# Kernel tuning notes

Measured on AMD Instinct MI355X. Metric: run time of the kernel, lower is better.

Reference implementation:

```python
import jax, jax.numpy as jnp
import numpy as np

N_NODES = 100000
N_EDGES = 150000
D_IN = 512
D_HID = 512
N_GRAPHS = 64


def setup_inputs() -> dict:
    key = jax.random.key(0)
    ks = jax.random.split(key, 12)
    x = jax.random.normal(ks[0], (N_NODES, D_IN), dtype=jnp.float32)
    edge_index = jax.random.randint(ks[1], (2, N_EDGES), 0, N_NODES, dtype=jnp.int64)
    batch = jnp.sort(jax.random.randint(ks[2], (N_NODES,), 0, N_GRAPHS, dtype=jnp.int64))
    s1 = 1.0 / np.sqrt(D_IN)
    s2 = 1.0 / np.sqrt(D_HID)
    # GINConv layer 1: MLP([D_IN, D_HID, D_HID])
    W1a = jax.random.uniform(ks[3], (D_IN, D_HID), jnp.float32, -s1, s1)
    b1a = jax.random.uniform(ks[4], (D_HID,), jnp.float32, -s1, s1)
    W1b = jax.random.uniform(ks[5], (D_HID, D_HID), jnp.float32, -s2, s2)
    b1b = jax.random.uniform(ks[6], (D_HID,), jnp.float32, -s2, s2)
    # GINConv layer 2 (out_channels=1): MLP([D_HID, 1, 1])
    W2a = jax.random.uniform(ks[7], (D_HID, 1), jnp.float32, -s2, s2)
    b2a = jax.random.uniform(ks[8], (1,), jnp.float32, -s2, s2)
    W2b = jax.random.uniform(ks[9], (1, 1), jnp.float32, -1.0, 1.0)
    b2b = jax.random.uniform(ks[10], (1,), jnp.float32, -1.0, 1.0)
    return {"x": x, "edge_index": edge_index, "batch": batch,
            "W1a": W1a, "b1a": b1a, "W1b": W1b, "b1b": b1b,
            "W2a": W2a, "b2a": b2a, "W2b": W2b, "b2b": b2b}


def _gin_conv(h, src, dst, Wa, ba, Wb, bb):
    # sum-aggregate neighbor features, add (1+eps)*x with eps=0, then MLP
    agg = jax.ops.segment_sum(h[src], dst, num_segments=N_NODES)  # [N, d]
    z = agg + h
    z = jnp.maximum(jnp.dot(z, Wa) + ba, 0.0)  # Linear -> ReLU
    return jnp.dot(z, Wb) + bb                  # Linear (plain last)


def reference(x, edge_index, batch, W1a, b1a, W1b, b1b, W2a, b2a, W2b, b2b):
    src, dst = edge_index[0], edge_index[1]
    h = _gin_conv(x, src, dst, W1a, b1a, W1b, b1b)
    h = jnp.maximum(h, 0.0)  # inter-layer activation (not applied after last layer)
    h = _gin_conv(h, src, dst, W2a, b2a, W2b, b2b)  # [N, 1]
    # global mean pool over graph assignment
    sums = jax.ops.segment_sum(h, batch, num_segments=N_GRAPHS)  # [G, 1]
    cnt = jax.ops.segment_sum(jnp.ones((N_NODES, 1), h.dtype), batch, num_segments=N_GRAPHS)
    return sums / jnp.maximum(cnt, 1.0)
```

## Files before the change

### kernel.cpp

```cpp
#include <hip/hip_runtime.h>
#include <hip/hip_bf16.h>

#define N_NODES_C 100000
#define N_EDGES_C 150000
#define DC 512
#define NG 64

typedef float f32x4 __attribute__((ext_vector_type(4)));
typedef short s16x8 __attribute__((ext_vector_type(8)));
typedef unsigned int u32;

__device__ __forceinline__ short f2bf(float f) {
    union { float f; unsigned u; } c; c.f = f;
    unsigned r = c.u + 0x7fffu + ((c.u >> 16) & 1u);
    return (short)(r >> 16);
}
__device__ __forceinline__ float bf2f(short v) {
    union { unsigned u; float f; } c;
    c.u = ((unsigned)(unsigned short)v) << 16;
    return c.f;
}

__device__ __forceinline__ void gload16(const void* g, void* l) {
    __builtin_amdgcn_global_load_lds((const __attribute__((address_space(1))) u32*)g,
                                     (__attribute__((address_space(3))) u32*)l,
                                     16, 0, 0);
}


__global__ void zero_k(float* s, float* aggs, int* cnt, float* gsum, float* gcnt) {
    int i = blockIdx.x * 256 + threadIdx.x;
    if (i < N_NODES_C) { s[i] = 0.f; aggs[i] = 0.f; cnt[i] = 0; }
    if (i < NG) { gsum[i] = 0.f; gcnt[i] = 0.f; }
}

__global__ void transpose_w(const float* __restrict__ in, short* __restrict__ out) {
    __shared__ float tile[32][33];
    int tx = threadIdx.x & 31;
    int ty = threadIdx.x >> 5;
    int k0 = blockIdx.y * 32;
    int n0 = blockIdx.x * 32;
#pragma unroll
    for (int i = 0; i < 4; ++i)
        tile[ty + i * 8][tx] = in[(size_t)(k0 + ty + i * 8) * DC + n0 + tx];
    __syncthreads();
#pragma unroll
    for (int i = 0; i < 4; ++i)
        out[(size_t)(n0 + ty + i * 8) * DC + k0 + tx] = f2bf(tile[tx][ty + i * 8]);
}


__global__ void hist_k(const int* __restrict__ ei, int* __restrict__ cnt) {
    int e = blockIdx.x * 256 + threadIdx.x;
    if (e < N_EDGES_C) atomicAdd(&cnt[ei[N_EDGES_C + e]], 1);
}

__global__ void scan1_k(const int* __restrict__ cnt, int* __restrict__ off,
                        int* __restrict__ bsum) {
    __shared__ int sh[1024];
    int tid = threadIdx.x;
    int i = blockIdx.x * 1024 + tid;
    int v = (i < N_NODES_C) ? cnt[i] : 0;
    sh[tid] = v;
    __syncthreads();
    for (int d = 1; d < 1024; d <<= 1) {
        int t = (tid >= d) ? sh[tid - d] : 0;
        __syncthreads();
        sh[tid] += t;
        __syncthreads();
    }
    if (i < N_NODES_C) off[i] = sh[tid] - v;
    if (tid == 1023) bsum[blockIdx.x] = sh[1023];
}

#define NSCAN_BLK 98

__global__ void scan2_k(int* __restrict__ bsum) {
    __shared__ int sh[128];
    int tid = threadIdx.x;
    int v = (tid < NSCAN_BLK) ? bsum[tid] : 0;
    sh[tid] = v;
    __syncthreads();
    for (int d = 1; d < 128; d <<= 1) {
        int t = (tid >= d) ? sh[tid - d] : 0;
        __syncthreads();
        sh[tid] += t;
        __syncthreads();
    }
    if (tid < NSCAN_BLK) bsum[tid] = sh[tid] - v;
}

__global__ void scan3_k(int* __restrict__ off, const int* __restrict__ bsum) {
    int i = blockIdx.x * 1024 + threadIdx.x;
    if (i < N_NODES_C) off[i] += bsum[blockIdx.x];
}

__global__ void place_k(const int* __restrict__ ei, int* __restrict__ off,
                        int* __restrict__ ssrc) {
    int e = blockIdx.x * 256 + threadIdx.x;
    if (e < N_EDGES_C) {
        int d = ei[N_EDGES_C + e];
        int p = atomicAdd(&off[d], 1);
        ssrc[p] = ei[e];
    }
}

__global__ void gather_relu_k(const short* __restrict__ y, const int* __restrict__ off,
                              const int* __restrict__ ssrc, const float* __restrict__ b1a,
                              short* __restrict__ z1) {
    int node = blockIdx.x * 4 + (threadIdx.x >> 6);
    if (node >= N_NODES_C) return;
    int t = threadIdx.x & 63;
    const int col = t * 8;
    int beg = (node == 0) ? 0 : off[node - 1];
    int end = off[node];
    s16x8 own = *(const s16x8*)(y + (size_t)node * DC + col);
    float acc[8];
#pragma unroll
    for (int q = 0; q < 8; ++q) acc[q] = bf2f(own[q]);
    int j = beg;
    for (; j + 2 <= end; j += 2) {
        int s0 = ssrc[j];
        int s1 = ssrc[j + 1];
        s16x8 r0 = *(const s16x8*)(y + (size_t)s0 * DC + col);
        s16x8 r1 = *(const s16x8*)(y + (size_t)s1 * DC + col);
#pragma unroll
        for (int q = 0; q < 8; ++q) acc[q] += bf2f(r0[q]) + bf2f(r1[q]);
    }
    if (j < end) {
        int s0 = ssrc[j];
        s16x8 r0 = *(const s16x8*)(y + (size_t)s0 * DC + col);
#pragma unroll
        for (int q = 0; q < 8; ++q) acc[q] += bf2f(r0[q]);
    }
    f32x4 bv0 = *(const f32x4*)(b1a + col);
    f32x4 bv1 = *(const f32x4*)(b1a + col + 4);
    s16x8 o;
    o[0] = f2bf(fmaxf(acc[0] + bv0.x, 0.f));
    o[1] = f2bf(fmaxf(acc[1] + bv0.y, 0.f));
    o[2] = f2bf(fmaxf(acc[2] + bv0.z, 0.f));
    o[3] = f2bf(fmaxf(acc[3] + bv0.w, 0.f));
    o[4] = f2bf(fmaxf(acc[4] + bv1.x, 0.f));
    o[5] = f2bf(fmaxf(acc[5] + bv1.y, 0.f));
    o[6] = f2bf(fmaxf(acc[6] + bv1.z, 0.f));
    o[7] = f2bf(fmaxf(acc[7] + bv1.w, 0.f));
    *(s16x8*)(z1 + (size_t)node * DC + col) = o;
}


__global__ void edge_scalar(const int* __restrict__ ei, const float* __restrict__ s,
                            float* __restrict__ aggs) {
    int e = blockIdx.x * 256 + threadIdx.x;
    if (e < N_EDGES_C) atomicAdd(&aggs[ei[N_EDGES_C + e]], s[ei[e]]);
}

__global__ void node_pool(const float* __restrict__ s, const float* __restrict__ aggs,
                          const int* __restrict__ batch, const float* __restrict__ b2a,
                          float* __restrict__ gsum, float* __restrict__ gcnt) {
    __shared__ float ls[NG], lc[NG];
    int t = threadIdx.x;
    if (t < NG) { ls[t] = 0.f; lc[t] = 0.f; }
    __syncthreads();
    int i = blockIdx.x * 256 + t;
    if (i < N_NODES_C) {
        float z2 = fmaxf(aggs[i] + s[i] + b2a[0], 0.0f);
        int g = batch[i];
        atomicAdd(&ls[g], z2);
        atomicAdd(&lc[g], 1.0f);
    }
    __syncthreads();
    if (t < NG && lc[t] != 0.f) {
        atomicAdd(&gsum[t], ls[t]);
        atomicAdd(&gcnt[t], lc[t]);
    }
}

__global__ void finalize_k(const float* gsum, const float* gcnt, const float* w2b,
                           const float* b2b, float* out) {
    int g = threadIdx.x;
    if (g < NG) {
        float c = fmaxf(gcnt[g], 1.0f);
        out[g] = gsum[g] / c * w2b[0] + b2b[0];
    }
}

#define BM 128
#define BN 128
#define BK 32
#define NKT (DC / BK)
#define NRB 782
#define NCB 4
#define NWG (NRB * NCB)
#define WG_PER_XCD (NWG / 8)

template <int ASRC, int EPI>
__global__ __launch_bounds__(256, 3) void gemm_k(const void* __restrict__ Ap,
                                                 const short* __restrict__ Bt,
                                                 const float* __restrict__ bias,
                                                 short* __restrict__ Cout,
                                                 const float* __restrict__ w2a,
                                                 float* __restrict__ s_out) {
    __shared__ alignas(16) short As[BM * BK];
    __shared__ alignas(16) short Bs[BN * BK];

    const int tid = threadIdx.x;
    const int bid = blockIdx.x;
    const int lin = (bid & 7) * WG_PER_XCD + (bid >> 3);
    const int brow = (lin >> 2) * BM;
    const int bcol = (lin & 3) * BN;

    const int w    = tid >> 6;
    const int lane = tid & 63;
    const int wr   = (w >> 1) * 64;
    const int wc   = (w & 1) * 64;
    const int lr   = lane & 15;
    const int lk   = (lane >> 4) * 8;

    f32x4 acc[4][4] = {};

    const int srow = lane >> 2;
    const int scol = (lane & 3) * 8;
    const short* bg0 = Bt + (size_t)(bcol + w * 32 + srow) * DC + scol;
    const short* bg1 = bg0 + (size_t)16 * DC;
    short* bl0 = &Bs[(w * 32) * BK];
    short* bl1 = &Bs[(w * 32 + 16) * BK];

    const short* ag0 = nullptr;
    const short* ag1 = nullptr;
    short* al0 = nullptr;
    short* al1 = nullptr;
    const float* af32 = nullptr;
    f32x4 areg[4];
    const int awrow = tid >> 1;
    const int awcol = (tid & 1) * 16;

    if constexpr (ASRC == 1) {
        int ar0 = brow + w * 32 + srow;
        int ar1 = ar0 + 16;
        if (ar0 >= N_NODES_C) ar0 = N_NODES_C - 1;
        if (ar1 >= N_NODES_C) ar1 = N_NODES_C - 1;
        ag0 = (const short*)Ap + (size_t)ar0 * DC + scol;
        ag1 = (const short*)Ap + (size_t)ar1 * DC + scol;
        al0 = &As[(w * 32) * BK];
        al1 = &As[(w * 32 + 16) * BK];
    } else {
        int ar = brow + awrow;
        if (ar >= N_NODES_C) ar = N_NODES_C - 1;
        af32 = (const float*)Ap + (size_t)ar * DC + awcol;
#pragma unroll
        for (int q = 0; q < 4; ++q) areg[q] = *(const f32x4*)(af32 + q * 4);
    }

    for (int kt = 0; kt < NKT; ++kt) {
        const int k0 = kt * BK;
        __syncthreads();
        if constexpr (ASRC == 1) {
            gload16(ag0 + k0, al0);
            gload16(ag1 + k0, al1);
        } else {
            s16x8 c0, c1;
            c0[0] = f2bf(areg[0].x); c0[1] = f2bf(areg[0].y);
            c0[2] = f2bf(areg[0].z); c0[3] = f2bf(areg[0].w);
            c0[4] = f2bf(areg[1].x); c0[5] = f2bf(areg[1].y);
            c0[6] = f2bf(areg[1].z); c0[7] = f2bf(areg[1].w);
            c1[0] = f2bf(areg[2].x); c1[1] = f2bf(areg[2].y);
            c1[2] = f2bf(areg[2].z); c1[3] = f2bf(areg[2].w);
            c1[4] = f2bf(areg[3].x); c1[5] = f2bf(areg[3].y);
            c1[6] = f2bf(areg[3].z); c1[7] = f2bf(areg[3].w);
            *(s16x8*)&As[awrow * BK + awcol + 0] = c0;
            *(s16x8*)&As[awrow * BK + awcol + 8] = c1;
        }
        gload16(bg0 + k0, bl0);
        gload16(bg1 + k0, bl1);
        __syncthreads();

        if constexpr (ASRC == 0) {
            if (kt + 1 < NKT) {
#pragma unroll
                for (int q = 0; q < 4; ++q)
                    areg[q] = *(const f32x4*)(af32 + (kt + 1) * BK + q * 4);
            }
        }

        s16x8 af[4], bfr[4];
#pragma unroll
        for (int mi = 0; mi < 4; ++mi)
            af[mi] = *(const s16x8*)&As[(wr + mi * 16 + lr) * BK + lk];
#pragma unroll
        for (int ni = 0; ni < 4; ++ni)
            bfr[ni] = *(const s16x8*)&Bs[(wc + ni * 16 + lr) * BK + lk];
        __builtin_amdgcn_s_setprio(1);
#pragma unroll
        for (int mi = 0; mi < 4; ++mi)
#pragma unroll
            for (int ni = 0; ni < 4; ++ni)
                acc[mi][ni] = __builtin_amdgcn_mfma_f32_16x16x32_bf16(af[mi], bfr[ni],
                                                                      acc[mi][ni], 0, 0, 0);
        __builtin_amdgcn_s_setprio(0);
    }

    const int rb = brow + wr + (lane >> 4) * 4;
    const int cb = bcol + wc + lr;

    if constexpr (EPI == 2) {
#pragma unroll
        for (int mi = 0; mi < 4; ++mi) {
#pragma unroll
            for (int r = 0; r < 4; ++r) {
                int row = rb + mi * 16 + r;
                if (row < N_NODES_C) {
#pragma unroll
                    for (int ni = 0; ni < 4; ++ni)
                        Cout[(size_t)row * DC + cb + ni * 16] = f2bf(acc[mi][ni][r]);
                }
            }
        }
    } else {
        float bv[4], wv[4];
#pragma unroll
        for (int ni = 0; ni < 4; ++ni) {
            bv[ni] = bias[cb + ni * 16];
            wv[ni] = w2a[cb + ni * 16];
        }
#pragma unroll
        for (int mi = 0; mi < 4; ++mi) {
#pragma unroll
            for (int r = 0; r < 4; ++r) {
                float sum = 0.f;
#pragma unroll
                for (int ni = 0; ni < 4; ++ni) {
                    float v = fmaxf(acc[mi][ni][r] + bv[ni], 0.0f);
                    sum += v * wv[ni];
                }
#pragma unroll
                for (int off = 1; off < 16; off <<= 1) sum += __shfl_xor(sum, off, 64);
                int row = rb + mi * 16 + r;
                if (lr == 0 && row < N_NODES_C) atomicAdd(&s_out[row], sum);
            }
        }
    }
}


extern "C" void kernel_launch(void* const* d_in, const int* in_sizes, int n_in,
                              void* d_out, int out_size, void* d_ws, size_t ws_size,
                              hipStream_t stream) {
    const float* x     = (const float*)d_in[0];
    const int*   ei    = (const int*)d_in[1];
    const int*   batch = (const int*)d_in[2];
    const float* W1a   = (const float*)d_in[3];
    const float* b1a   = (const float*)d_in[4];
    const float* W1b   = (const float*)d_in[5];
    const float* b1b   = (const float*)d_in[6];
    const float* W2a   = (const float*)d_in[7];
    const float* b2a   = (const float*)d_in[8];
    const float* W2b   = (const float*)d_in[9];
    const float* b2b   = (const float*)d_in[10];
    float* out = (float*)d_out;

    char* w = (char*)d_ws;
    short* z1   = (short*)(w);
    short* y    = (short*)(w + 102400000);
    short* WT1  = (short*)(w + 204800000);
    short* WT2  = (short*)(w + 205324288);
    float* sbuf = (float*)(w + 205848576);
    float* aggs = (float*)(w + 206248576);
    int*   cnt  = (int*)  (w + 206648576);
    int*   offb = (int*)  (w + 207048576);
    int*   ssrc = (int*)  (w + 207448576);
    int*   bsum = (int*)  (w + 208048576);
    float* gsum = (float*)(w + 208049088);
    float* gcnt = (float*)(w + 208049344);

    zero_k<<<391, 256, 0, stream>>>(sbuf, aggs, cnt, gsum, gcnt);
    transpose_w<<<dim3(16, 16), 256, 0, stream>>>(W1a, WT1);
    transpose_w<<<dim3(16, 16), 256, 0, stream>>>(W1b, WT2);

    hist_k<<<586, 256, 0, stream>>>(ei, cnt);
    scan1_k<<<NSCAN_BLK, 1024, 0, stream>>>(cnt, offb, bsum);
    scan2_k<<<1, 128, 0, stream>>>(bsum);
    scan3_k<<<NSCAN_BLK, 1024, 0, stream>>>(offb, bsum);
    place_k<<<586, 256, 0, stream>>>(ei, offb, ssrc);

    gemm_k<0, 2><<<NWG, 256, 0, stream>>>(x, WT1, nullptr, y, nullptr, nullptr);
    gather_relu_k<<<25000, 256, 0, stream>>>(y, offb, ssrc, b1a, z1);
    gemm_k<1, 1><<<NWG, 256, 0, stream>>>(z1, WT2, b1b, nullptr, W2a, sbuf);

    edge_scalar<<<586, 256, 0, stream>>>(ei, sbuf, aggs);
    node_pool<<<391, 256, 0, stream>>>(sbuf, aggs, batch, b2a, gsum, gcnt);
    finalize_k<<<1, 64, 0, stream>>>(gsum, gcnt, W2b, b2b, out);
}
```

Before: 297.4 us.

## Rewrite GEMM with 256x128 tiles, triple-buffered LDS and swizzled layout

Replaces the 128x128x32 double-sync GEMM with a 512-thread kernel using 256x128 tiles, BK=64, and a three-stage LDS ring buffer that prefetches two K-tiles ahead. Waits use explicit vmcnt counts and a single barrier per iteration. The LDS layout is XOR-swizzled to avoid bank conflicts. This is meant to hide global-load latency and cut barrier overhead, at the cost of 144KB of dynamic LDS, which limits occupancy to one workgroup per CU, plus hand-tuned waitcnt logic that is fragile.

```diff
diff --git a/kernel.cpp b/kernel.cpp
--- a/kernel.cpp
+++ b/kernel.cpp
@@ -184,123 +184,191 @@
     }
 }
 
-#define BM 128
-#define BN 128
-#define BK 32
-#define NKT (DC / BK)
-#define NRB 782
-#define NCB 4
-#define NWG (NRB * NCB)
-#define WG_PER_XCD (NWG / 8)
+#define NKT8 8
+#define BUF_SHORTS 24576
+#define LDS_BYTES (3 * BUF_SHORTS * 2)
+#define NWG8 1568
+#define WPX8 196
+
+#define VMCNT(n) asm volatile("s_waitcnt vmcnt(" #n ")")
+#define LGKM0() asm volatile("s_waitcnt lgkmcnt(0)")
+#define SCHEDB() __builtin_amdgcn_sched_barrier(0)
+#define HWBAR() __builtin_amdgcn_s_barrier()
 
 template <int ASRC, int EPI>
-__global__ __launch_bounds__(256, 3) void gemm_k(const void* __restrict__ Ap,
-                                                 const short* __restrict__ Bt,
-                                                 const float* __restrict__ bias,
-                                                 short* __restrict__ Cout,
-                                                 const float* __restrict__ w2a,
-                                                 float* __restrict__ s_out) {
-    __shared__ alignas(16) short As[BM * BK];
-    __shared__ alignas(16) short Bs[BN * BK];
+__global__ __launch_bounds__(512) void gemm8_k(const void* __restrict__ Ap,
+                                               const short* __restrict__ Bt,
+                                               const float* __restrict__ bias,
+                                               short* __restrict__ Cout,
+                                               const float* __restrict__ w2a,
+                                               float* __restrict__ s_out) {
+    extern __shared__ short lds[];
 
     const int tid = threadIdx.x;
     const int bid = blockIdx.x;
-    const int lin = (bid & 7) * WG_PER_XCD + (bid >> 3);
-    const int brow = (lin >> 2) * BM;
-    const int bcol = (lin & 3) * BN;
+    const int lin = (bid & 7) * WPX8 + (bid >> 3);
+    const int brow = (lin >> 2) * 256;
+    const int bcol = (lin & 3) * 128;
 
     const int w    = tid >> 6;
     const int lane = tid & 63;
-    const int wr   = (w >> 1) * 64;
-    const int wc   = (w & 1) * 64;
+    const int wm   = w >> 1;
+    const int wn   = w & 1;
     const int lr   = lane & 15;
-    const int lk   = (lane >> 4) * 8;
+    const int lg   = lane >> 4;
+    const int l3   = lane >> 3;
+    const int sc   = ((lane & 7) ^ l3) * 8;
 
     f32x4 acc[4][4] = {};
 
-    const int srow = lane >> 2;
-    const int scol = (lane & 3) * 8;
-    const short* bg0 = Bt + (size_t)(bcol + w * 32 + srow) * DC + scol;
-    const short* bg1 = bg0 + (size_t)16 * DC;
-    short* bl0 = &Bs[(w * 32) * BK];
-    short* bl1 = &Bs[(w * 32 + 16) * BK];
-
-    const short* ag0 = nullptr;
-    const short* ag1 = nullptr;
-    short* al0 = nullptr;
-    short* al1 = nullptr;
-    const float* af32 = nullptr;
-    f32x4 areg[4];
-    const int awrow = tid >> 1;
-    const int awcol = (tid & 1) * 16;
-
+    const short* bsrc0 = Bt + (size_t)(bcol + 0 * 64 + w * 8 + l3) * DC + sc;
+    const short* bsrc1 = Bt + (size_t)(bcol + 1 * 64 + w * 8 + l3) * DC + sc;
+    const int boff0 = 16384 + (0 * 64 + w * 8) * 64;
+    const int boff1 = 16384 + (1 * 64 + w * 8) * 64;
+
+    const short* asrc[4];
+    int aoff[4];
+    const float* axsrc = nullptr;
+    int awoff[4];
     if constexpr (ASRC == 1) {
-        int ar0 = brow + w * 32 + srow;
-        int ar1 = ar0 + 16;
-        if (ar0 >= N_NODES_C) ar0 = N_NODES_C - 1;
-        if (ar1 >= N_NODES_C) ar1 = N_NODES_C - 1;
-        ag0 = (const short*)Ap + (size_t)ar0 * DC + scol;
-        ag1 = (const short*)Ap + (size_t)ar1 * DC + scol;
-        al0 = &As[(w * 32) * BK];
-        al1 = &As[(w * 32 + 16) * BK];
+#pragma unroll
+        for (int i = 0; i < 4; ++i) {
+            int r = brow + i * 64 + w * 8 + l3;
+            if (r >= N_NODES_C) r = N_NODES_C - 1;
+            asrc[i] = (const short*)Ap + (size_t)r * DC + sc;
+            aoff[i] = (i * 64 + w * 8) * 64;
+        }
     } else {
-        int ar = brow + awrow;
-        if (ar >= N_NODES_C) ar = N_NODES_C - 1;
-        af32 = (const float*)Ap + (size_t)ar * DC + awcol;
-#pragma unroll
-        for (int q = 0; q < 4; ++q) areg[q] = *(const f32x4*)(af32 + q * 4);
-    }
-
-    for (int kt = 0; kt < NKT; ++kt) {
-        const int k0 = kt * BK;
-        __syncthreads();
-        if constexpr (ASRC == 1) {
-            gload16(ag0 + k0, al0);
-            gload16(ag1 + k0, al1);
+        const int rAl = tid >> 1;
+        int r = brow + rAl;
+        if (r >= N_NODES_C) r = N_NODES_C - 1;
+        axsrc = (const float*)Ap + (size_t)r * DC + (tid & 1) * 32;
+#pragma unroll
+        for (int j = 0; j < 4; ++j)
+            awoff[j] = rAl * 64 + ((((tid & 1) * 4 + j) ^ (rAl & 7)) * 8);
+    }
+
+#define STAGE_B(t, sb_)                                  \
+    do {                                                 \
+        short* _p = &lds[(sb_)*BUF_SHORTS];              \
+        gload16(bsrc0 + (t)*64, _p + boff0);             \
+        gload16(bsrc1 + (t)*64, _p + boff1);             \
+    } while (0)
+#define STAGE_A1(t, sb_)                                 \
+    do {                                                 \
+        short* _p = &lds[(sb_)*BUF_SHORTS];              \
+        gload16(asrc[0] + (t)*64, _p + aoff[0]);         \
+        gload16(asrc[1] + (t)*64, _p + aoff[1]);         \
+        gload16(asrc[2] + (t)*64, _p + aoff[2]);         \
+        gload16(asrc[3] + (t)*64, _p + aoff[3]);         \
+    } while (0)
+#define LOAD_A0(t, fr)                                                    \
+    _Pragma("unroll") for (int q = 0; q < 8; ++q)                         \
+        fr[q] = *(const f32x4*)(axsrc + (t)*64 + q * 4);
+#define WRITE_A0(sb_, fr)                                                 \
+    do {                                                                  \
+        short* _p = &lds[(sb_)*BUF_SHORTS];                               \
+        _Pragma("unroll") for (int j = 0; j < 4; ++j) {                   \
+            s16x8 _c;                                                     \
+            _c[0] = f2bf(fr[2 * j].x);     _c[1] = f2bf(fr[2 * j].y);     \
+            _c[2] = f2bf(fr[2 * j].z);     _c[3] = f2bf(fr[2 * j].w);     \
+            _c[4] = f2bf(fr[2 * j + 1].x); _c[5] = f2bf(fr[2 * j + 1].y); \
+            _c[6] = f2bf(fr[2 * j + 1].z); _c[7] = f2bf(fr[2 * j + 1].w); \
+            *(s16x8*)&_p[awoff[j]] = _c;                                  \
+        }                                                                 \
+    } while (0)
+
+    if constexpr (ASRC == 1) {
+        STAGE_A1(0, 0); STAGE_B(0, 0);
+        STAGE_A1(1, 1); STAGE_B(1, 1);
+        VMCNT(6);
+        SCHEDB();
+        HWBAR();
+    } else {
+        f32x4 p0[8], p1[8];
+        LOAD_A0(0, p0);
+        STAGE_B(0, 0);
+        LOAD_A0(1, p1);
+        STAGE_B(1, 1);
+        WRITE_A0(0, p0);
+        WRITE_A0(1, p1);
+        VMCNT(0);
+        LGKM0();
+        SCHEDB();
+        HWBAR();
+    }
+
+    int bufR = 0, bufS = 2;
+    for (int kt = 0; kt < NKT8; ++kt) {
+        const short* bp = &lds[bufR * BUF_SHORTS];
+
+        f32x4 fr[8];
+        if (kt < NKT8 - 2) {
+            if constexpr (ASRC == 1) {
+                STAGE_A1(kt + 2, bufS);
+                STAGE_B(kt + 2, bufS);
+            } else {
+                LOAD_A0(kt + 2, fr);
+                STAGE_B(kt + 2, bufS);
+            }
+            SCHEDB();
+        }
+
+#pragma unroll
+        for (int kk = 0; kk < 2; ++kk) {
+            s16x8 af[4], bfr[4];
+#pragma unroll
+            for (int mi = 0; mi < 4; ++mi)
+                af[mi] = *(const s16x8*)&bp[(wm * 64 + mi * 16 + lr) * 64 +
+                                            (((kk * 4 + lg) ^ (lr & 7)) * 8)];
+#pragma unroll
+            for (int ni = 0; ni < 4; ++ni)
+                bfr[ni] = *(const s16x8*)&bp[16384 + (wn * 64 + ni * 16 + lr) * 64 +
+                                             (((kk * 4 + lg) ^ (lr & 7)) * 8)];
+            __builtin_amdgcn_s_setprio(1);
+#pragma unroll
+            for (int mi = 0; mi < 4; ++mi)
+#pragma unroll
+                for (int ni = 0; ni < 4; ++ni)
+                    acc[mi][ni] = __builtin_amdgcn_mfma_f32_16x16x32_bf16(
+                        af[mi], bfr[ni], acc[mi][ni], 0, 0, 0);
+            __builtin_amdgcn_s_setprio(0);
+        }
+
+        if constexpr (ASRC == 0) {
+            if (kt < NKT8 - 2) {
+                VMCNT(2);
+                SCHEDB();
+                WRITE_A0(bufS, fr);
+                LGKM0();
+                SCHEDB();
+                HWBAR();
+            } else if (kt == NKT8 - 2) {
+                VMCNT(0);
+                SCHEDB();
+                HWBAR();
+            }
         } else {
-            s16x8 c0, c1;
-            c0[0] = f2bf(areg[0].x); c0[1] = f2bf(areg[0].y);
-            c0[2] = f2bf(areg[0].z); c0[3] = f2bf(areg[0].w);
-            c0[4] = f2bf(areg[1].x); c0[5] = f2bf(areg[1].y);
-            c0[6] = f2bf(areg[1].z); c0[7] = f2bf(areg[1].w);
-            c1[0] = f2bf(areg[2].x); c1[1] = f2bf(areg[2].y);
-            c1[2] = f2bf(areg[2].z); c1[3] = f2bf(areg[2].w);
-            c1[4] = f2bf(areg[3].x); c1[5] = f2bf(areg[3].y);
-            c1[6] = f2bf(areg[3].z); c1[7] = f2bf(areg[3].w);
-            *(s16x8*)&As[awrow * BK + awcol + 0] = c0;
-            *(s16x8*)&As[awrow * BK + awcol + 8] = c1;
-        }
-        gload16(bg0 + k0, bl0);
-        gload16(bg1 + k0, bl1);
-        __syncthreads();
-
-        if constexpr (ASRC == 0) {
-            if (kt + 1 < NKT) {
-#pragma unroll
-                for (int q = 0; q < 4; ++q)
-                    areg[q] = *(const f32x4*)(af32 + (kt + 1) * BK + q * 4);
+            if (kt < NKT8 - 2) {
+                VMCNT(6);
+                SCHEDB();
+                HWBAR();
+            } else if (kt == NKT8 - 2) {
+                VMCNT(0);
+                SCHEDB();
+                HWBAR();
             }
         }
-
-        s16x8 af[4], bfr[4];
-#pragma unroll
-        for (int mi = 0; mi < 4; ++mi)
-            af[mi] = *(const s16x8*)&As[(wr + mi * 16 + lr) * BK + lk];
-#pragma unroll
-        for (int ni = 0; ni < 4; ++ni)
-            bfr[ni] = *(const s16x8*)&Bs[(wc + ni * 16 + lr) * BK + lk];
-        __builtin_amdgcn_s_setprio(1);
-#pragma unroll
-        for (int mi = 0; mi < 4; ++mi)
-#pragma unroll
-            for (int ni = 0; ni < 4; ++ni)
-                acc[mi][ni] = __builtin_amdgcn_mfma_f32_16x16x32_bf16(af[mi], bfr[ni],
-                                                                      acc[mi][ni], 0, 0, 0);
-        __builtin_amdgcn_s_setprio(0);
-    }
-
-    const int rb = brow + wr + (lane >> 4) * 4;
-    const int cb = bcol + wc + lr;
+        bufR = (bufR == 2) ? 0 : bufR + 1;
+        bufS = (bufS == 2) ? 0 : bufS + 1;
+    }
+#undef STAGE_B
+#undef STAGE_A1
+#undef LOAD_A0
+#undef WRITE_A0
+
+    const int rb = brow + wm * 64 + lg * 4;
+    const int cb = bcol + wn * 64 + lr;
 
     if constexpr (EPI == 2) {
 #pragma unroll
@@ -372,6 +440,11 @@
     float* gsum = (float*)(w + 208049088);
     float* gcnt = (float*)(w + 208049344);
 
+    hipFuncSetAttribute(reinterpret_cast<const void*>(&gemm8_k<0, 2>),
+                        hipFuncAttributeMaxDynamicSharedMemorySize, LDS_BYTES);
+    hipFuncSetAttribute(reinterpret_cast<const void*>(&gemm8_k<1, 1>),
+                        hipFuncAttributeMaxDynamicSharedMemorySize, LDS_BYTES);
+
     zero_k<<<391, 256, 0, stream>>>(sbuf, aggs, cnt, gsum, gcnt);
     transpose_w<<<dim3(16, 16), 256, 0, stream>>>(W1a, WT1);
     transpose_w<<<dim3(16, 16), 256, 0, stream>>>(W1b, WT2);
@@ -382,9 +455,9 @@
     scan3_k<<<NSCAN_BLK, 1024, 0, stream>>>(offb, bsum);
     place_k<<<586, 256, 0, stream>>>(ei, offb, ssrc);
 
-    gemm_k<0, 2><<<NWG, 256, 0, stream>>>(x, WT1, nullptr, y, nullptr, nullptr);
+    gemm8_k<0, 2><<<NWG8, 512, LDS_BYTES, stream>>>(x, WT1, nullptr, y, nullptr, nullptr);
     gather_relu_k<<<25000, 256, 0, stream>>>(y, offb, ssrc, b1a, z1);
-    gemm_k<1, 1><<<NWG, 256, 0, stream>>>(z1, WT2, b1b, nullptr, W2a, sbuf);
+    gemm8_k<1, 1><<<NWG8, 512, LDS_BYTES, stream>>>(z1, WT2, b1b, nullptr, W2a, sbuf);
 
     edge_scalar<<<586, 256, 0, stream>>>(ei, sbuf, aggs);
     node_pool<<<391, 256, 0, stream>>>(sbuf, aggs, batch, b2a, gsum, gcnt);
```

Result: slower. 375.9 us (+26.4%).

## Double GEMM K-tile to 64 with XOR-swizzled LDS layout and higher occupancy

Applied to the files above, without the earlier changes.

Raises the GEMM K tile from 32 to 64, which halves the number of barrier-separated k-iterations. It adds an XOR swizzle on the LDS A/B tiles so the wider rows avoid bank conflicts on the fragment reads, and raises launch bounds to 4 waves per EU. The f32 A path now holds 8 vector registers of prefetch instead of 4, which adds register pressure and LDS use per block against the occupancy target.

```diff
diff --git a/kernel.cpp b/kernel.cpp
--- a/kernel.cpp
+++ b/kernel.cpp
@@ -186,15 +186,13 @@
 
 #define BM 128
 #define BN 128
-#define BK 32
+#define BK 64
 #define NKT (DC / BK)
-#define NRB 782
-#define NCB 4
-#define NWG (NRB * NCB)
-#define WG_PER_XCD (NWG / 8)
+#define NWG 3128
+#define WPX 391
 
 template <int ASRC, int EPI>
-__global__ __launch_bounds__(256, 3) void gemm_k(const void* __restrict__ Ap,
+__global__ __launch_bounds__(256, 4) void gemm_k(const void* __restrict__ Ap,
                                                  const short* __restrict__ Bt,
                                                  const float* __restrict__ bias,
                                                  short* __restrict__ Cout,
@@ -205,7 +203,7 @@
 
     const int tid = threadIdx.x;
     const int bid = blockIdx.x;
-    const int lin = (bid & 7) * WG_PER_XCD + (bid >> 3);
+    const int lin = (bid & 7) * WPX + (bid >> 3);
     const int brow = (lin >> 2) * BM;
     const int bcol = (lin & 3) * BN;
 
@@ -214,92 +212,94 @@
     const int wr   = (w >> 1) * 64;
     const int wc   = (w & 1) * 64;
     const int lr   = lane & 15;
-    const int lk   = (lane >> 4) * 8;
+    const int lg   = lane >> 4;
 
     f32x4 acc[4][4] = {};
 
-    const int srow = lane >> 2;
-    const int scol = (lane & 3) * 8;
-    const short* bg0 = Bt + (size_t)(bcol + w * 32 + srow) * DC + scol;
-    const short* bg1 = bg0 + (size_t)16 * DC;
-    short* bl0 = &Bs[(w * 32) * BK];
-    short* bl1 = &Bs[(w * 32 + 16) * BK];
-
-    const short* ag0 = nullptr;
-    const short* ag1 = nullptr;
-    short* al0 = nullptr;
-    short* al1 = nullptr;
-    const float* af32 = nullptr;
-    f32x4 areg[4];
-    const int awrow = tid >> 1;
-    const int awcol = (tid & 1) * 16;
-
+    const int l8 = lane >> 3;
+    const int scs = ((lane & 7) ^ l8) * 8;
+
+    const short* bsrc = Bt + (size_t)(bcol + w * 32 + l8) * DC + scs;
+    const short* asrc[4];
+    const float* axsrc = nullptr;
+    int awoff[4];
+    const int rAl = tid >> 1;
     if constexpr (ASRC == 1) {
-        int ar0 = brow + w * 32 + srow;
-        int ar1 = ar0 + 16;
-        if (ar0 >= N_NODES_C) ar0 = N_NODES_C - 1;
-        if (ar1 >= N_NODES_C) ar1 = N_NODES_C - 1;
-        ag0 = (const short*)Ap + (size_t)ar0 * DC + scol;
-        ag1 = (const short*)Ap + (size_t)ar1 * DC + scol;
-        al0 = &As[(w * 32) * BK];
-        al1 = &As[(w * 32 + 16) * BK];
+#pragma unroll
+        for (int j = 0; j < 4; ++j) {
+            int r = brow + w * 32 + j * 8 + l8;
+            if (r >= N_NODES_C) r = N_NODES_C - 1;
+            asrc[j] = (const short*)Ap + (size_t)r * DC + scs;
+        }
     } else {
-        int ar = brow + awrow;
-        if (ar >= N_NODES_C) ar = N_NODES_C - 1;
-        af32 = (const float*)Ap + (size_t)ar * DC + awcol;
-#pragma unroll
-        for (int q = 0; q < 4; ++q) areg[q] = *(const f32x4*)(af32 + q * 4);
+        int r = brow + rAl;
+        if (r >= N_NODES_C) r = N_NODES_C - 1;
+        axsrc = (const float*)Ap + (size_t)r * DC + (tid & 1) * 32;
+#pragma unroll
+        for (int j = 0; j < 4; ++j)
+            awoff[j] = rAl * BK + ((((tid & 1) * 4 + j) ^ (rAl & 7)) * 8);
+    }
+
+    f32x4 areg[8];
+    if constexpr (ASRC == 0) {
+#pragma unroll
+        for (int q = 0; q < 8; ++q) areg[q] = *(const f32x4*)(axsrc + q * 4);
     }
 
     for (int kt = 0; kt < NKT; ++kt) {
         const int k0 = kt * BK;
         __syncthreads();
         if constexpr (ASRC == 1) {
-            gload16(ag0 + k0, al0);
-            gload16(ag1 + k0, al1);
+#pragma unroll
+            for (int j = 0; j < 4; ++j)
+                gload16(asrc[j] + j * 8 * DC + k0, &As[(w * 32 + j * 8) * BK]);
         } else {
-            s16x8 c0, c1;
-            c0[0] = f2bf(areg[0].x); c0[1] = f2bf(areg[0].y);
-            c0[2] = f2bf(areg[0].z); c0[3] = f2bf(areg[0].w);
-            c0[4] = f2bf(areg[1].x); c0[5] = f2bf(areg[1].y);
-            c0[6] = f2bf(areg[1].z); c0[7] = f2bf(areg[1].w);
-            c1[0] = f2bf(areg[2].x); c1[1] = f2bf(areg[2].y);
-            c1[2] = f2bf(areg[2].z); c1[3] = f2bf(areg[2].w);
-            c1[4] = f2bf(areg[3].x); c1[5] = f2bf(areg[3].y);
-            c1[6] = f2bf(areg[3].z); c1[7] = f2bf(areg[3].w);
-            *(s16x8*)&As[awrow * BK + awcol + 0] = c0;
-            *(s16x8*)&As[awrow * BK + awcol + 8] = c1;
-        }
-        gload16(bg0 + k0, bl0);
-        gload16(bg1 + k0, bl1);
+#pragma unroll
+            for (int j = 0; j < 4; ++j) {
+                s16x8 c;
+                c[0] = f2bf(areg[2 * j].x);     c[1] = f2bf(areg[2 * j].y);
+                c[2] = f2bf(areg[2 * j].z);     c[3] = f2bf(areg[2 * j].w);
+                c[4] = f2bf(areg[2 * j + 1].x); c[5] = f2bf(areg[2 * j + 1].y);
+                c[6] = f2bf(areg[2 * j + 1].z); c[7] = f2bf(areg[2 * j + 1].w);
+                *(s16x8*)&As[awoff[j]] = c;
+            }
+        }
+#pragma unroll
+        for (int j = 0; j < 4; ++j)
+            gload16(bsrc + j * 8 * DC + k0, &Bs[(w * 32 + j * 8) * BK]);
         __syncthreads();
 
         if constexpr (ASRC == 0) {
             if (kt + 1 < NKT) {
 #pragma unroll
-                for (int q = 0; q < 4; ++q)
-                    areg[q] = *(const f32x4*)(af32 + (kt + 1) * BK + q * 4);
+                for (int q = 0; q < 8; ++q)
+                    areg[q] = *(const f32x4*)(axsrc + (kt + 1) * BK + q * 4);
             }
         }
 
-        s16x8 af[4], bfr[4];
-#pragma unroll
-        for (int mi = 0; mi < 4; ++mi)
-            af[mi] = *(const s16x8*)&As[(wr + mi * 16 + lr) * BK + lk];
-#pragma unroll
-        for (int ni = 0; ni < 4; ++ni)
-            bfr[ni] = *(const s16x8*)&Bs[(wc + ni * 16 + lr) * BK + lk];
-        __builtin_amdgcn_s_setprio(1);
-#pragma unroll
-        for (int mi = 0; mi < 4; ++mi)
+#pragma unroll
+        for (int kk = 0; kk < 2; ++kk) {
+            s16x8 af[4], bfr[4];
+#pragma unroll
+            for (int mi = 0; mi < 4; ++mi)
+                af[mi] = *(const s16x8*)&As[(wr + mi * 16 + lr) * BK +
+                                            (((kk * 4 + lg) ^ (lr & 7)) * 8)];
 #pragma unroll
             for (int ni = 0; ni < 4; ++ni)
-                acc[mi][ni] = __builtin_amdgcn_mfma_f32_16x16x32_bf16(af[mi], bfr[ni],
-                                                                      acc[mi][ni], 0, 0, 0);
-        __builtin_amdgcn_s_setprio(0);
-    }
-
-    const int rb = brow + wr + (lane >> 4) * 4;
+                bfr[ni] = *(const s16x8*)&Bs[(wc + ni * 16 + lr) * BK +
+                                             (((kk * 4 + lg) ^ (lr & 7)) * 8)];
+            __builtin_amdgcn_s_setprio(1);
+#pragma unroll
+            for (int mi = 0; mi < 4; ++mi)
+#pragma unroll
+                for (int ni = 0; ni < 4; ++ni)
+                    acc[mi][ni] = __builtin_amdgcn_mfma_f32_16x16x32_bf16(
+                        af[mi], bfr[ni], acc[mi][ni], 0, 0, 0);
+            __builtin_amdgcn_s_setprio(0);
+        }
+    }
+
+    const int rb = brow + wr + lg * 4;
     const int cb = bcol + wc + lr;
 
     if constexpr (EPI == 2) {
```

After: 431.3 us. 1.45x slower.
